# Kernel optimization log

Hardware: AMD Instinct MI355X
Metric: run time of the kernel (lower is better)

The kernel has to match this reference:

```python
import jax, jax.numpy as jnp
import numpy as np

B_SZ, C, H, W = 64, 256, 28, 28
HEADS, HEAD_DIM = 4, 64
BLOCK, HALO = 4, 4
WIN = BLOCK + 2 * HALO  # 12
KCONV = 3


def _unfold(x, k, s, p):
    # torch F.unfold semantics; returns [b, c, oh, kh, ow, kw]
    b, c, h, w = x.shape
    xp = jnp.pad(x, ((0, 0), (0, 0), (p, p), (p, p)))
    oh = (h + 2 * p - k) // s + 1
    ow = (w + 2 * p - k) // s + 1
    ih = jnp.arange(oh)[:, None] * s + jnp.arange(k)[None, :]
    iw = jnp.arange(ow)[:, None] * s + jnp.arange(k)[None, :]
    pt = xp[:, :, ih]            # [b,c,oh,kh,Wp]
    pt = pt[:, :, :, :, iw]      # [b,c,oh,kh,ow,kw]
    return pt


def _rel_to_abs(x):
    # x: [b, l, 2r-1] -> [b, l, r] via shift trick
    b, l, m = x.shape
    r = (m + 1) // 2
    x = jnp.pad(x, ((0, 0), (0, 0), (0, 1))).reshape(b, l * (m + 1))
    x = jnp.pad(x, ((0, 0), (0, m - l))).reshape(b, l + 1, m)
    return x[:, :l, -r:]


def _relative_logits_1d(q, rel_k):
    # q: [b, x, y, d], rel_k: [2r-1, d] -> [b, x, i(=r), y, j(=r)]
    b, h, w, _ = q.shape
    r = (rel_k.shape[0] + 1) // 2
    logits = jnp.einsum('bxyd,rd->bxyr', q, rel_k)
    logits = _rel_to_abs(logits.reshape(b * h, w, 2 * r - 1)).reshape(b, h, w, r)
    return jnp.broadcast_to(logits[:, :, None], (b, h, r, w, r))


def _rel_pos_emb(q, rel_height, rel_width):
    # q: [B, block^2, d]
    B, n, d = q.shape
    qb = q.reshape(B, BLOCK, BLOCK, d)
    lw = _relative_logits_1d(qb, rel_width)                 # [B,x,i,y,j]
    lw = lw.transpose(0, 1, 3, 2, 4).reshape(B, n, -1)      # b (x y) (i j)
    qh = qb.transpose(0, 2, 1, 3)
    lh = _relative_logits_1d(qh, rel_height)                # [B,y,i,x,j]
    lh = lh.transpose(0, 3, 1, 4, 2).reshape(B, n, -1)      # b (y x) (j i)
    return lw + lh


def setup_inputs() -> dict:
    key = jax.random.key(0)
    ks = jax.random.split(key, 13)
    f = jnp.float32
    rel_scale = HEAD_DIM ** (-0.5)
    return {
        'x': jax.random.normal(ks[0], (B_SZ, C, H, W), dtype=f),
        'w1': jax.random.normal(ks[1], (C, C), dtype=f) * 0.05,
        'b1': jax.random.normal(ks[2], (C,), dtype=f) * 0.05,
        'w2': jax.random.normal(ks[3], (C, C), dtype=f) * 0.05,
        'b2': jax.random.normal(ks[4], (C,), dtype=f) * 0.05,
        'w3': jax.random.normal(ks[5], (C, C), dtype=f) * 0.05,
        'b3': jax.random.normal(ks[6], (C,), dtype=f) * 0.05,
        'fc_w': jax.random.normal(ks[7], (KCONV * KCONV, 3 * HEADS), dtype=f) * 0.1,
        'dep_w': jax.random.normal(ks[8], (C, KCONV * KCONV, KCONV, KCONV), dtype=f) * 0.05,
        'rel_height': jax.random.normal(ks[9], (2 * WIN - 1, HEAD_DIM), dtype=f) * rel_scale,
        'rel_width': jax.random.normal(ks[10], (2 * WIN - 1, HEAD_DIM), dtype=f) * rel_scale,
        'rate1': jax.random.normal(ks[11], (1,), dtype=f),
        'rate2': jax.random.normal(ks[12], (1,), dtype=f),
    }


def reference(x, w1, b1, w2, b2, w3, b3, fc_w, dep_w, rel_height, rel_width, rate1, rate2):
    b = x.shape[0]
    scaling = HEAD_DIM ** (-0.5)
    q = jnp.einsum('bchw,oc->bohw', x, w1) + b1[None, :, None, None]
    k = jnp.einsum('bchw,oc->bohw', x, w2) + b2[None, :, None, None]
    v = jnp.einsum('bchw,oc->bohw', x, w3) + b3[None, :, None, None]
    c = q.shape[1]
    nb = H // BLOCK          # 7 blocks per side
    nwin = nb * nb           # 49 windows
    n_q = BLOCK * BLOCK      # 16 queries per window
    n_k = WIN * WIN          # 144 keys per window (with halo)

    # block queries: b c (h p1) (w p2) -> (b h w) (p1 p2) c
    q_att = q.reshape(b, c, nb, BLOCK, nb, BLOCK).transpose(0, 2, 4, 3, 5, 1).reshape(b * nwin, n_q, c)
    kp = _unfold(k, WIN, BLOCK, HALO).transpose(0, 2, 4, 3, 5, 1).reshape(b * nwin, n_k, c)
    vp = _unfold(v, WIN, BLOCK, HALO).transpose(0, 2, 4, 3, 5, 1).reshape(b * nwin, n_k, c)

    def split_heads(t):
        Bn, n, _ = t.shape
        return t.reshape(Bn, n, HEADS, HEAD_DIM).transpose(0, 2, 1, 3).reshape(Bn * HEADS, n, HEAD_DIM)

    q1 = split_heads(q_att) * scaling
    k1 = split_heads(kp)
    v1 = split_heads(vp)

    sim = jnp.einsum('bid,bjd->bij', q1, k1)
    sim = sim + _rel_pos_emb(q1, rel_height, rel_width)

    # NOTE: faithfully reproduces original (valid positions get -max, padded get 0)
    ones = jnp.ones((1, 1, H, W), x.dtype)
    valid = _unfold(ones, WIN, BLOCK, HALO).transpose(0, 2, 4, 3, 5, 1).reshape(nwin, n_k) > 0
    big_neg = -jnp.finfo(sim.dtype).max
    sim = sim.reshape(b, nwin, HEADS, n_q, n_k)
    sim = jnp.where(valid[None, :, None, None, :], big_neg, sim)
    attn = jax.nn.softmax(sim, axis=-1).reshape(b * nwin * HEADS, n_q, n_k)

    out = jnp.einsum('bij,bjd->bid', attn, v1)
    out = out.reshape(b * nwin, HEADS, n_q, HEAD_DIM).transpose(0, 2, 1, 3)  # merge heads
    out = out.reshape(b, nb, nb, BLOCK, BLOCK, c)
    out_att = out.transpose(0, 5, 1, 3, 2, 4).reshape(b, c, H, W)

    # conv branch: fc over concatenated per-head q,k,v, then depthwise-grouped conv
    f_all = jnp.concatenate([
        q.reshape(b, HEADS, HEAD_DIM, H * W),
        k.reshape(b, HEADS, HEAD_DIM, H * W),
        v.reshape(b, HEADS, HEAD_DIM, H * W)], axis=1)        # [b, 3*heads, hd, HW]
    f_all = jnp.einsum('bcmn,oc->bomn', f_all, fc_w)          # [b, 9, hd, HW]
    f_conv = f_all.transpose(0, 2, 1, 3).reshape(b, HEAD_DIM * KCONV * KCONV, H, W)
    out_conv = jax.lax.conv_general_dilated(
        f_conv, dep_w, window_strides=(1, 1), padding=((1, 1), (1, 1)),
        dimension_numbers=('NCHW', 'OIHW', 'NCHW'), feature_group_count=HEAD_DIM)

    return rate1[0] * out_att + rate2[0] * out_conv
```

## Files before the change

kernel.cpp:

```cpp
#include <hip/hip_runtime.h>
#include <hip/hip_bf16.h>

typedef __hip_bfloat16 bf16;
typedef unsigned int uint;
typedef unsigned short ushort;

using frag8 = __attribute__((ext_vector_type(8))) short;
using f32x4 = __attribute__((ext_vector_type(4))) float;

#define HWH 784
#define PPITCH 30
#define PPLANE 900
#define PBLK 10800

__global__ __launch_bounds__(256) void fold_w2(const float* __restrict__ fc_w,
                                               const float* __restrict__ dep_w,
                                               const float* __restrict__ b1,
                                               const float* __restrict__ b2,
                                               const float* __restrict__ b3,
                                               float* __restrict__ W2,
                                               float* __restrict__ biascat) {
    int idx = blockIdx.x * 256 + threadIdx.x;
    if (idx < 768) {
        const float* bs = idx < 256 ? b1 : (idx < 512 ? b2 : b3);
        biascat[idx] = bs[idx & 255];
    }
    if (idx >= 256 * 108) return;
    int oc  = idx / 108;
    int r   = idx % 108;
    int c12 = r / 9;
    int k9  = r % 9;
    float s = 0.f;
#pragma unroll
    for (int o = 0; o < 9; ++o)
        s += fc_w[o * 12 + c12] * dep_w[oc * 81 + o * 9 + k9];
    W2[idx] = s;
}

__global__ __launch_bounds__(256) void wprep(const float* __restrict__ w1,
                                             const float* __restrict__ w2,
                                             const float* __restrict__ w3,
                                             bf16* __restrict__ wbf) {
    int row = blockIdx.x, tid = threadIdx.x;
    const float* src = row < 256 ? w1 : (row < 512 ? w2 : w3);
    wbf[row * 256 + tid] = __float2bfloat16(src[(row & 255) * 256 + tid]);
}

__global__ __launch_bounds__(256) void xpose(const float* __restrict__ x,
                                             bf16* __restrict__ xT) {
    __shared__ float t[32][33];
    const int n0 = blockIdx.x * 32, c0 = blockIdx.y * 32, b = blockIdx.z;
    const int tid = threadIdx.x;
    const float* xb = x + (size_t)b * (256 * HWH);
#pragma unroll
    for (int e = tid; e < 1024; e += 256) {
        int r = e >> 5, col = e & 31;
        int n = n0 + col;
        t[r][col] = (n < HWH) ? xb[(size_t)(c0 + r) * HWH + n] : 0.f;
    }
    __syncthreads();
#pragma unroll
    for (int e = tid; e < 512; e += 256) {
        int r = e >> 4, cp = (e & 15) * 2;
        int n = n0 + r;
        if (n < HWH) {
            __hip_bfloat162 h;
            h.x = __float2bfloat16(t[cp][r]);
            h.y = __float2bfloat16(t[cp + 1][r]);
            *reinterpret_cast<__hip_bfloat162*>(
                &xT[((size_t)b * HWH + n) * 256 + c0 + cp]) = h;
        }
    }
}

__device__ inline void load_lds16(const bf16* g, short* lds) {
    __builtin_amdgcn_global_load_lds(
        (const __attribute__((address_space(1))) void*)g,
        (__attribute__((address_space(3))) void*)lds, 16, 0, 0);
}

__global__ __launch_bounds__(256) void gemm_mfma(const bf16* __restrict__ wbf,
                                                 const float* __restrict__ biascat,
                                                 const bf16* __restrict__ xT,
                                                 bf16* __restrict__ perm) {
    __shared__ short lds[8192];

    const int tid  = threadIdx.x;
    const int wave = tid >> 6, lane = tid & 63;
    const int b    = blockIdx.z;
    const int m0   = blockIdx.y * 128;
    const int n0   = blockIdx.x * 128;
    const int mw   = wave & 1, nw = wave >> 1;
    const int lrow = lane & 15, lkc = lane >> 4;

    f32x4 acc[4][4] = {};
    const bf16* xb = xT + (size_t)b * (HWH * 256);

    for (int k0 = 0; k0 < 256; k0 += 32) {
#pragma unroll
        for (int i = 0; i < 2; ++i) {
            const int jb = 2 * wave + i;
            const bf16* ga = wbf + (size_t)(m0 + 16 * jb + lrow) * 256 + k0 + lkc * 8;
            load_lds16(ga, &lds[jb * 512]);
            int n = n0 + 16 * jb + lrow;
            if (n > HWH - 1) n = HWH - 1;
            const bf16* gb = xb + (size_t)n * 256 + k0 + lkc * 8;
            load_lds16(gb, &lds[4096 + jb * 512]);
        }
        __syncthreads();

        frag8 af[4], bf_[4];
#pragma unroll
        for (int i = 0; i < 4; ++i)
            af[i] = *reinterpret_cast<const frag8*>(&lds[(4 * mw + i) * 512 + lane * 8]);
#pragma unroll
        for (int j = 0; j < 4; ++j)
            bf_[j] = *reinterpret_cast<const frag8*>(&lds[4096 + (4 * nw + j) * 512 + lane * 8]);
#pragma unroll
        for (int i = 0; i < 4; ++i)
#pragma unroll
            for (int j = 0; j < 4; ++j)
                acc[i][j] = __builtin_amdgcn_mfma_f32_16x16x32_bf16(
                    af[i], bf_[j], acc[i][j], 0, 0, 0);
        __syncthreads();
    }

#pragma unroll
    for (int i = 0; i < 4; ++i) {
        const int rowb = m0 + mw * 64 + i * 16 + lkc * 4;
        bf16* base[4]; float bias4[4];
#pragma unroll
        for (int r = 0; r < 4; ++r) {
            const int m = rowb + r;
            const int sec = m >> 8, ch = m & 255;
            base[r] = perm + ((size_t)b * 64 + (ch & 63)) * PBLK
                           + (size_t)(sec * 4 + (ch >> 6)) * PPLANE;
            bias4[r] = biascat[m];
        }
#pragma unroll
        for (int j = 0; j < 4; ++j) {
            const int col = n0 + nw * 64 + j * 16 + lrow;
            if (col < HWH) {
                const int pos = col + 2 * (col / 28) + 31;
#pragma unroll
                for (int r = 0; r < 4; ++r)
                    base[r][pos] = __float2bfloat16(acc[i][j][r] + bias4[r]);
            }
        }
    }
}

__global__ __launch_bounds__(256) void attmean(const bf16* __restrict__ perm,
                                               const float* __restrict__ rate1,
                                               float* __restrict__ attm) {
    const int b = blockIdx.y, cg = blockIdx.x;
    const int wave = threadIdx.x >> 6, lane = threadIdx.x & 63;
    const int c = cg * 4 + wave;
    const bf16* vp = perm + ((size_t)(b * 64 + (c & 63)) * 12 + 8 + (c >> 6)) * (size_t)PPLANE;

    float cs[5] = {0.f, 0.f, 0.f, 0.f, 0.f};
    if (lane < 28) {
#pragma unroll
        for (int y = 0; y < 28; ++y) {
            float v = __bfloat162float(vp[(y + 1) * PPITCH + lane + 1]);
#pragma unroll
            for (int wi = 0; wi < 5; ++wi)
                if (y >= 4 * wi && y <= 4 * wi + 11) cs[wi] += v;
        }
    }
    const float r1s = rate1[0] * (1.0f / 144.0f);
#pragma unroll
    for (int wi = 0; wi < 5; ++wi) {
        float p = cs[wi];
#pragma unroll
        for (int d = 1; d < 32; d <<= 1) {
            float t = __shfl_up(p, d);
            if (lane >= d) p += t;
        }
        float hi = __shfl(p, 4 * lane + 11);
        float lo = __shfl(p, 4 * lane - 1);
        if (lane < 5) {
            float w = hi - (lane ? lo : 0.f);
            attm[((size_t)b * 256 + c) * 25 + wi * 5 + lane] = w * r1s;
        }
    }
}

__global__ __launch_bounds__(256) void out_fused5(
    const bf16* __restrict__ perm, const float* __restrict__ W2,
    const float* __restrict__ attm, const float* __restrict__ rate2,
    float* __restrict__ out) {
    __shared__ __align__(16) short planes[12 * PPLANE];
    __shared__ float w2s[4][12][12];
    __shared__ float attbs[4][25];

    const int g = blockIdx.x, b = blockIdx.y, tid = threadIdx.x;

    const uint4* src = (const uint4*)(perm + (size_t)(b * 64 + g) * PBLK);
#pragma unroll
    for (int it = 0; it < 6; ++it) {
        int e = tid + it * 256;
        if (e < 1350) ((uint4*)planes)[e] = src[e];
    }
    for (int e = tid; e < 576; e += 256) {
        int oc = e / 144, rem = e % 144, cc = rem / 12, k = rem % 12;
        w2s[oc][cc][k] = (k < 9) ? W2[(4 * g + oc) * 108 + cc * 9 + k] : 0.f;
    }
    if (tid < 100)
        attbs[tid / 25][tid % 25] =
            attm[((size_t)b * 256 + 4 * g + tid / 25) * 25 + tid % 25];
    __syncthreads();

    for (int e = tid; e < 1392; e += 256) {
        int c12 = e / 116, u = e % 116, idx;
        if (u < 30)      idx = u;
        else if (u < 60) idx = 870 + (u - 30);
        else { int v = u - 60; idx = ((v >> 1) + 1) * PPITCH + (v & 1) * 29; }
        planes[c12 * PPLANE + idx] = 0;
    }
    __syncthreads();

    float acc[4][4] = {};
    const int y = tid % 28, xs = tid / 28, x0 = xs * 4;
    if (tid < 196) {
#pragma unroll 1
        for (int c = 0; c < 12; ++c) {
            float rr[3][6];
#pragma unroll
            for (int dy = 0; dy < 3; ++dy) {
                const uint* row = (const uint*)&planes[c * PPLANE + (y + dy) * PPITCH + x0];
#pragma unroll
                for (int jp = 0; jp < 3; ++jp) {
                    uint w = row[jp];
                    float2 f = __bfloat1622float2(*(const __hip_bfloat162*)&w);
                    rr[dy][2 * jp]     = f.x;
                    rr[dy][2 * jp + 1] = f.y;
                }
            }
#pragma unroll
            for (int oc = 0; oc < 4; ++oc) {
                const float4* wr = reinterpret_cast<const float4*>(&w2s[oc][c][0]);
                float4 wa = wr[0], wb = wr[1], wc = wr[2];
                const float wk[9] = {wa.x, wa.y, wa.z, wa.w, wb.x, wb.y, wb.z, wb.w, wc.x};
#pragma unroll
                for (int ky = 0; ky < 3; ++ky)
#pragma unroll
                    for (int kx = 0; kx < 3; ++kx) {
                        float wv = wk[ky * 3 + kx];
#pragma unroll
                        for (int px = 0; px < 4; ++px)
                            acc[oc][px] += wv * rr[ky][px + kx];
                    }
            }
        }

        const float r2 = rate2[0];
        const int wi = (y >> 2) - 1, wj = xs - 1;
        const bool inter = (wi >= 0) & (wi < 5) & (wj >= 0) & (wj < 5);
#pragma unroll
        for (int oc = 0; oc < 4; ++oc) {
            float av = inter ? attbs[oc][wi * 5 + wj] : 0.f;
            float4 o;
            o.x = av + r2 * acc[oc][0];
            o.y = av + r2 * acc[oc][1];
            o.z = av + r2 * acc[oc][2];
            o.w = av + r2 * acc[oc][3];
            *reinterpret_cast<float4*>(
                &out[((size_t)(b * 256 + 4 * g + oc)) * HWH + y * 28 + x0]) = o;
        }
    }
}

extern "C" void kernel_launch(void* const* d_in, const int* in_sizes, int n_in,
                              void* d_out, int out_size, void* d_ws, size_t ws_size,
                              hipStream_t stream) {
    const float* x     = (const float*)d_in[0];
    const float* w1    = (const float*)d_in[1];
    const float* b1    = (const float*)d_in[2];
    const float* w2    = (const float*)d_in[3];
    const float* b2    = (const float*)d_in[4];
    const float* w3    = (const float*)d_in[5];
    const float* b3    = (const float*)d_in[6];
    const float* fc_w  = (const float*)d_in[7];
    const float* dep_w = (const float*)d_in[8];
    const float* rate1 = (const float*)d_in[11];
    const float* rate2 = (const float*)d_in[12];
    float* out = (float*)d_out;

    char* wsb = (char*)d_ws;
    bf16*  perm    = (bf16*)wsb;
    bf16*  xT      = (bf16*)(wsb + 88473600);
    float* attm    = (float*)(wsb + 88473600);
    bf16*  wbf     = (bf16*)(wsb + 114163712);
    float* W2      = (float*)(wsb + 114556928);
    float* biascat = (float*)(wsb + 114667520);

    fold_w2   <<<dim3(108),        dim3(256), 0, stream>>>(fc_w, dep_w, b1, b2, b3, W2, biascat);
    wprep     <<<dim3(768),        dim3(256), 0, stream>>>(w1, w2, w3, wbf);
    xpose     <<<dim3(25, 8, 64),  dim3(256), 0, stream>>>(x, xT);
    gemm_mfma <<<dim3(7, 6, 64),   dim3(256), 0, stream>>>(wbf, biascat, xT, perm);
    attmean   <<<dim3(64, 64),     dim3(256), 0, stream>>>(perm, rate1, attm);
    out_fused5<<<dim3(64, 64),     dim3(256), 0, stream>>>(perm, W2, attm, rate2, out);
}
```

Baseline: 256.7 us.

## Keep a full-K activation tile in LDS and loop over all output rows per block

The GEMM now gives each block a 64-column slice of one batch's activations. It loads the whole K=256 slice into LDS once and then loops over all 768 weight rows in six 128-row chunks, reading the weight fragments straight from global memory. This removes the per-k-step LDS staging and barriers, and the activation tile is read once per block instead of once per row-tile block. In exchange, weight reads go to global memory or cache on every chunk, the grid is smaller, and each wave holds fewer accumulators.

```diff
diff --git a/kernel.cpp b/kernel.cpp
--- a/kernel.cpp
+++ b/kernel.cpp
@@ -83,68 +83,71 @@
                                                  const float* __restrict__ biascat,
                                                  const bf16* __restrict__ xT,
                                                  bf16* __restrict__ perm) {
-    __shared__ short lds[8192];
+    __shared__ short ldsB[16384];
 
     const int tid  = threadIdx.x;
     const int wave = tid >> 6, lane = tid & 63;
-    const int b    = blockIdx.z;
-    const int m0   = blockIdx.y * 128;
-    const int n0   = blockIdx.x * 128;
-    const int mw   = wave & 1, nw = wave >> 1;
+    const int b    = blockIdx.y;
+    const int n0   = blockIdx.x * 64;
     const int lrow = lane & 15, lkc = lane >> 4;
 
-    f32x4 acc[4][4] = {};
     const bf16* xb = xT + (size_t)b * (HWH * 256);
 
-    for (int k0 = 0; k0 < 256; k0 += 32) {
+#pragma unroll
+    for (int si = 0; si < 8; ++si) {
+        const int s = wave * 8 + si;
+        const int kc = s >> 2, jb = s & 3;
+        int n = n0 + jb * 16 + lrow;
+        if (n > HWH - 1) n = HWH - 1;
+        const bf16* gb = xb + (size_t)n * 256 + kc * 32 + lkc * 8;
+        load_lds16(gb, &ldsB[s * 512]);
+    }
+    __syncthreads();
+
+#pragma unroll 1
+    for (int mt = 0; mt < 6; ++mt) {
+        f32x4 acc[2][4] = {};
+        const int rowbase = mt * 128 + wave * 32 + lrow;
+#pragma unroll 2
+        for (int kc = 0; kc < 8; ++kc) {
+            frag8 a[2], bb[4];
+#pragma unroll
+            for (int i = 0; i < 2; ++i)
+                a[i] = *reinterpret_cast<const frag8*>(
+                    &wbf[(size_t)(rowbase + i * 16) * 256 + kc * 32 + lkc * 8]);
+#pragma unroll
+            for (int j = 0; j < 4; ++j)
+                bb[j] = *reinterpret_cast<const frag8*>(
+                    &ldsB[(kc * 4 + j) * 512 + lane * 8]);
+#pragma unroll
+            for (int i = 0; i < 2; ++i)
+#pragma unroll
+                for (int j = 0; j < 4; ++j)
+                    acc[i][j] = __builtin_amdgcn_mfma_f32_16x16x32_bf16(
+                        a[i], bb[j], acc[i][j], 0, 0, 0);
+        }
+
 #pragma unroll
         for (int i = 0; i < 2; ++i) {
-            const int jb = 2 * wave + i;
-            const bf16* ga = wbf + (size_t)(m0 + 16 * jb + lrow) * 256 + k0 + lkc * 8;
-            load_lds16(ga, &lds[jb * 512]);
-            int n = n0 + 16 * jb + lrow;
-            if (n > HWH - 1) n = HWH - 1;
-            const bf16* gb = xb + (size_t)n * 256 + k0 + lkc * 8;
-            load_lds16(gb, &lds[4096 + jb * 512]);
-        }
-        __syncthreads();
-
-        frag8 af[4], bf_[4];
-#pragma unroll
-        for (int i = 0; i < 4; ++i)
-            af[i] = *reinterpret_cast<const frag8*>(&lds[(4 * mw + i) * 512 + lane * 8]);
-#pragma unroll
-        for (int j = 0; j < 4; ++j)
-            bf_[j] = *reinterpret_cast<const frag8*>(&lds[4096 + (4 * nw + j) * 512 + lane * 8]);
-#pragma unroll
-        for (int i = 0; i < 4; ++i)
-#pragma unroll
-            for (int j = 0; j < 4; ++j)
-                acc[i][j] = __builtin_amdgcn_mfma_f32_16x16x32_bf16(
-                    af[i], bf_[j], acc[i][j], 0, 0, 0);
-        __syncthreads();
-    }
-
-#pragma unroll
-    for (int i = 0; i < 4; ++i) {
-        const int rowb = m0 + mw * 64 + i * 16 + lkc * 4;
-        bf16* base[4]; float bias4[4];
-#pragma unroll
-        for (int r = 0; r < 4; ++r) {
-            const int m = rowb + r;
-            const int sec = m >> 8, ch = m & 255;
-            base[r] = perm + ((size_t)b * 64 + (ch & 63)) * PBLK
-                           + (size_t)(sec * 4 + (ch >> 6)) * PPLANE;
-            bias4[r] = biascat[m];
-        }
-#pragma unroll
-        for (int j = 0; j < 4; ++j) {
-            const int col = n0 + nw * 64 + j * 16 + lrow;
-            if (col < HWH) {
-                const int pos = col + 2 * (col / 28) + 31;
-#pragma unroll
-                for (int r = 0; r < 4; ++r)
-                    base[r][pos] = __float2bfloat16(acc[i][j][r] + bias4[r]);
+            const int rowb = mt * 128 + wave * 32 + i * 16 + lkc * 4;
+            bf16* base[4]; float bias4[4];
+#pragma unroll
+            for (int r = 0; r < 4; ++r) {
+                const int m = rowb + r;
+                const int sec = m >> 8, ch = m & 255;
+                base[r] = perm + ((size_t)b * 64 + (ch & 63)) * PBLK
+                               + (size_t)(sec * 4 + (ch >> 6)) * PPLANE;
+                bias4[r] = biascat[m];
+            }
+#pragma unroll
+            for (int j = 0; j < 4; ++j) {
+                const int col = n0 + j * 16 + lrow;
+                if (col < HWH) {
+                    const int pos = col + 2 * (col / 28) + 31;
+#pragma unroll
+                    for (int r = 0; r < 4; ++r)
+                        base[r][pos] = __float2bfloat16(acc[i][j][r] + bias4[r]);
+                }
             }
         }
     }
@@ -298,7 +301,7 @@
     fold_w2   <<<dim3(108),        dim3(256), 0, stream>>>(fc_w, dep_w, b1, b2, b3, W2, biascat);
     wprep     <<<dim3(768),        dim3(256), 0, stream>>>(w1, w2, w3, wbf);
     xpose     <<<dim3(25, 8, 64),  dim3(256), 0, stream>>>(x, xT);
-    gemm_mfma <<<dim3(7, 6, 64),   dim3(256), 0, stream>>>(wbf, biascat, xT, perm);
+    gemm_mfma <<<dim3(13, 64),     dim3(256), 0, stream>>>(wbf, biascat, xT, perm);
     attmean   <<<dim3(64, 64),     dim3(256), 0, stream>>>(perm, rate1, attm);
     out_fused5<<<dim3(64, 64),     dim3(256), 0, stream>>>(perm, W2, attm, rate2, out);
 }
```

After: 274.5 us. 6.9% more time.
